# Kernel tuning notes

Measured on AMD Instinct MI355X. Metric: run time of the kernel, lower is better.

## Reference

```python
import jax, jax.numpy as jnp
import numpy as np

B, Cin, Cout = 2, 32, 16
D, H, W = 48, 64, 128
K = 3
EPS = 1e-5  # BatchNorm3d default eps


def setup_inputs() -> dict:
    key = jax.random.key(0)
    ks = jax.random.split(key, 6)
    return {
        "x": jax.random.normal(ks[0], (B, Cin, D, H, W), jnp.float32),
        "weight": jax.random.normal(ks[1], (Cout, Cin, K, K, K), jnp.float32) * 0.05,
        "gamma": jax.random.uniform(ks[2], (Cout,), jnp.float32, minval=0.5, maxval=1.5),
        "beta": jax.random.normal(ks[3], (Cout,), jnp.float32) * 0.1,
        "running_mean": jax.random.normal(ks[4], (Cout,), jnp.float32) * 0.1,
        "running_var": jax.random.uniform(ks[5], (Cout,), jnp.float32, minval=0.5, maxval=1.5),
    }


def _binarize(v):
    # forward: sign(v) in {-1, 0, +1}; backward (STE): hardtanh grad (pass-through on |v|<=1)
    clipped = jnp.clip(v, -1.0, 1.0)
    return clipped + jax.lax.stop_gradient(jnp.sign(v) - clipped)


def reference(x, weight, gamma, beta, running_mean, running_var):
    b, c, d, h, w = x.shape
    # trilinear upsample, scale (1,2,2), align_corners=False (half-pixel centers)
    x = jax.image.resize(x, (b, c, d, 2 * h, 2 * w), method="trilinear")
    # binarize activations and weights; XNOR-style per-output-channel scale alpha = mean|W|
    xb = _binarize(x)
    alpha = jnp.mean(jnp.abs(weight), axis=(1, 2, 3, 4), keepdims=True)  # [Cout,1,1,1,1]
    wb = _binarize(weight) * alpha
    y = jax.lax.conv_general_dilated(
        xb, wb,
        window_strides=(1, 1, 1),
        padding=[(1, 1), (1, 1), (1, 1)],
        dimension_numbers=("NCDHW", "OIDHW", "NCDHW"),
    )  # [B, Cout, D, 2H, 2W]
    # fused BatchNorm3d (inference form) + ReLU
    inv = gamma / jnp.sqrt(running_var + EPS)
    shift = beta - running_mean * inv
    y = y * inv[None, :, None, None, None] + shift[None, :, None, None, None]
    return jax.nn.relu(y)
```

## Files before the change

### kernel.cpp

```cpp
#include <hip/hip_runtime.h>
#include <hip/hip_bf16.h>
#include <stdint.h>

#define BB   2
#define CIN  32
#define COUT 16
#define DD   48
#define HIN  64
#define WIN  128
#define H2   128
#define W2   256
#define PLANE_WORDS (H2 * W2)

__global__ __launch_bounds__(512) void ibc3d_prep(
    const float* __restrict__ wgt, const float* __restrict__ gamma,
    const float* __restrict__ beta, const float* __restrict__ rmean,
    const float* __restrict__ rvar, uint32_t* __restrict__ bw,
    float* __restrict__ scale, float* __restrict__ shift)
{
    int t = threadIdx.x;
    if (t < 27 * 16) {
        int tap = t >> 4, co = t & 15;
        uint32_t word = 0;
        for (int ci = 0; ci < CIN; ++ci) {
            float v = wgt[(co * CIN + ci) * 27 + tap];
            word |= (v > 0.0f ? 1u : 0u) << ci;
        }
        bw[t] = word;
    } else if (t < 27 * 16 + 16) {
        int co = t - 27 * 16;
        double s = 0.0;
        for (int i = 0; i < CIN * 27; ++i)
            s += fabs((double)wgt[co * CIN * 27 + i]);
        float alpha = (float)(s / (double)(CIN * 27));
        float inv = gamma[co] / sqrtf(rvar[co] + 1e-5f);
        scale[co] = alpha * inv;
        shift[co] = beta[co] - rmean[co] * inv;
    }
}

__device__ __forceinline__ uint32_t pack_word(const float* __restrict__ x,
                                              int b, int d, int h2, int w2)
{
    int m = h2 >> 1, dh = h2 & 1;
    int n = w2 >> 1, dwp = w2 & 1;
    int rA = m + dh - 1;
    int rB = rA + 1;
    double wA = dh ? 0.75 : 0.25;
    double wB = 1.0 - wA;
    rA = rA < 0 ? 0 : rA;
    rB = rB > (HIN - 1) ? (HIN - 1) : rB;
    int cA = n + dwp - 1;
    int cB = cA + 1;
    double wC = dwp ? 0.75 : 0.25;
    double wD = 1.0 - wC;
    cA = cA < 0 ? 0 : cA;
    cB = cB > (WIN - 1) ? (WIN - 1) : cB;

    const float* xp = x + ((size_t)b * CIN * DD + d) * (HIN * WIN);
    int oA = rA * WIN, oB = rB * WIN;
    uint32_t word = 0;
    for (int ci = 0; ci < CIN; ++ci) {
        const float* xc = xp + (size_t)ci * (DD * HIN * WIN);
        float a0 = xc[oA + cA], a1 = xc[oA + cB];
        float b0 = xc[oB + cA], b1 = xc[oB + cB];
        double t0 = wA * (double)a0 + wB * (double)b0;
        double t1 = wA * (double)a1 + wB * (double)b1;
        double v  = wC * t0 + wD * t1;
        word |= (v >= 0.0 ? 1u : 0u) << ci;
    }
    return word;
}

__global__ __launch_bounds__(256) void ibc3d_packq8(
    const float* __restrict__ x, uint32_t* __restrict__ bx,
    int b_start, int nplanes)
{
    int idx = blockIdx.x * 256 + threadIdx.x;
    int j  = idx & 31;
    int m  = (idx >> 5) & 63;
    int pl = idx >> 11;
    if (pl >= nplanes) return;
    int d  = pl % DD;
    int b  = b_start + pl / DD;

    int rm1 = m > 0 ? m - 1 : 0;
    int rp1 = m < HIN - 1 ? m + 1 : HIN - 1;
    int c0  = 4 * j;
    int cl  = c0 >= 2 ? c0 - 2 : 0;
    int cr  = (c0 + 4 <= WIN - 2) ? c0 + 4 : WIN - 2;

    const float* xp = x + ((size_t)b * CIN * DD + d) * (HIN * WIN);
    int o0 = rm1 * WIN, o1 = m * WIN, o2 = rp1 * WIN;

    uint32_t w0[8], w1[8];
#pragma unroll
    for (int k = 0; k < 8; ++k) { w0[k] = 0u; w1[k] = 0u; }

#pragma unroll 2
    for (int ci = 0; ci < CIN; ++ci) {
        const float* xc = xp + (size_t)ci * (DD * HIN * WIN);
        float c[3][6];
#pragma unroll
        for (int r = 0; r < 3; ++r) {
            const float* row = xc + (r == 0 ? o0 : (r == 1 ? o1 : o2));
            float2 L = *(const float2*)(row + cl);
            float4 M = *(const float4*)(row + c0);
            float2 R = *(const float2*)(row + cr);
            c[r][0] = (j > 0)  ? L.y : L.x;
            c[r][1] = M.x; c[r][2] = M.y; c[r][3] = M.z; c[r][4] = M.w;
            c[r][5] = (j < 31) ? R.x : R.y;
        }

        float u[3][8];
#pragma unroll
        for (int r = 0; r < 3; ++r) {
#pragma unroll
            for (int t = 0; t < 4; ++t) {
                u[r][2 * t]     = 0.25f * c[r][t]     + 0.75f * c[r][t + 1];
                u[r][2 * t + 1] = 0.75f * c[r][t + 1] + 0.25f * c[r][t + 2];
            }
        }
        float v0[8], v1[8];
#pragma unroll
        for (int k = 0; k < 8; ++k) {
            v0[k] = 0.25f * u[0][k] + 0.75f * u[1][k];
            v1[k] = 0.75f * u[1][k] + 0.25f * u[2][k];
        }

        float amin = 3.4e38f;
#pragma unroll
        for (int k = 0; k < 8; ++k)
            amin = fminf(amin, fminf(fabsf(v0[k]), fabsf(v1[k])));

        if (__builtin_expect(amin < 1e-5f, 0)) {
            double e[3][8];
#pragma unroll
            for (int r = 0; r < 3; ++r) {
#pragma unroll
                for (int t = 0; t < 4; ++t) {
                    e[r][2 * t]     = 0.25 * (double)c[r][t]     + 0.75 * (double)c[r][t + 1];
                    e[r][2 * t + 1] = 0.75 * (double)c[r][t + 1] + 0.25 * (double)c[r][t + 2];
                }
            }
#pragma unroll
            for (int k = 0; k < 8; ++k) {
                uint32_t s0 = (0.25 * e[0][k] + 0.75 * e[1][k]) >= 0.0;
                uint32_t s1 = (0.75 * e[1][k] + 0.25 * e[2][k]) >= 0.0;
                w0[k] |= s0 << ci;
                w1[k] |= s1 << ci;
            }
        } else {
#pragma unroll
            for (int k = 0; k < 8; ++k) {
                uint32_t s0 = v0[k] >= 0.0f;
                uint32_t s1 = v1[k] >= 0.0f;
                w0[k] |= s0 << ci;
                w1[k] |= s1 << ci;
            }
        }
    }

    size_t base = (size_t)pl * PLANE_WORDS + (size_t)(2 * m) * W2 + 8 * j;
    *(uint4*)(bx + base)          = make_uint4(w0[0], w0[1], w0[2], w0[3]);
    *(uint4*)(bx + base + 4)      = make_uint4(w0[4], w0[5], w0[6], w0[7]);
    *(uint4*)(bx + base + W2)     = make_uint4(w1[0], w1[1], w1[2], w1[3]);
    *(uint4*)(bx + base + W2 + 4) = make_uint4(w1[4], w1[5], w1[6], w1[7]);
}

__global__ __launch_bounds__(256) void ibc3d_conv3(
    const uint32_t* __restrict__ bx, const uint32_t* __restrict__ bwg,
    const float* __restrict__ scaleg, const float* __restrict__ shiftg,
    float* __restrict__ out, int b_start)
{
    int bid   = blockIdx.x;
    int h2    = bid & (H2 - 1);
    int plane = bid >> 7;
    int d     = plane % DD;
    int b     = b_start + plane / DD;
    int w2    = threadIdx.x;

    int acc[16];
#pragma unroll
    for (int c = 0; c < 16; ++c) acc[c] = 0;

#pragma unroll
    for (int kd = 0; kd < 3; ++kd) {
        int dd = d + kd - 1;
        if (dd < 0 || dd >= DD) continue;
        const uint32_t* bxp = bx + (size_t)(plane + kd - 1) * PLANE_WORDS;
#pragma unroll
        for (int kh = 0; kh < 3; ++kh) {
            int hh = h2 + kh - 1;
            if (hh < 0 || hh >= H2) continue;
            const uint32_t* brow = bxp + hh * W2;
#pragma unroll
            for (int kw = 0; kw < 3; ++kw) {
                int ww = w2 + kw - 1;
                if (ww >= 0 && ww < W2) {
                    uint32_t word = brow[ww];
                    int tap = kd * 9 + kh * 3 + kw;
#pragma unroll
                    for (int co = 0; co < 16; ++co)
                        acc[co] += __popc(word ^ bwg[tap * 16 + co]);
                }
            }
        }
    }

    int nd = 1 + (d > 0)  + (d < DD - 1);
    int nh = 1 + (h2 > 0) + (h2 < H2 - 1);
    int nw = 1 + (w2 > 0) + (w2 < W2 - 1);
    float base = 32.0f * (float)(nd * nh * nw);

    size_t obase = (((size_t)(b * COUT) * DD + d) * H2 + h2) * W2 + w2;
#pragma unroll
    for (int co = 0; co < 16; ++co) {
        float y = (base - 2.0f * (float)acc[co]) * scaleg[co] + shiftg[co];
        y = y > 0.0f ? y : 0.0f;
        out[obase + (size_t)co * (DD * H2 * W2)] = y;
    }
}

__global__ __launch_bounds__(256) void ibc3d_fused(
    const float* __restrict__ x, const float* __restrict__ wgt,
    const float* __restrict__ gamma, const float* __restrict__ beta,
    const float* __restrict__ rmean, const float* __restrict__ rvar,
    float* __restrict__ out)
{
    __shared__ uint32_t sbw[27 * 16];
    __shared__ float sscale[16];
    __shared__ float sshift[16];
    __shared__ uint32_t sw[3][10][264];

    int tid = threadIdx.x;
    for (int t = tid; t < 27 * 16; t += 256) {
        int tap = t >> 4, co = t & 15;
        uint32_t word = 0;
        for (int ci = 0; ci < CIN; ++ci) {
            float v = wgt[(co * CIN + ci) * 27 + tap];
            word |= (v > 0.0f ? 1u : 0u) << ci;
        }
        sbw[t] = word;
    }
    if (tid < 16) {
        int co = tid;
        double s = 0.0;
        for (int i = 0; i < CIN * 27; ++i)
            s += fabs((double)wgt[co * CIN * 27 + i]);
        float alpha = (float)(s / (double)(CIN * 27));
        float inv = gamma[co] / sqrtf(rvar[co] + 1e-5f);
        sscale[co] = alpha * inv;
        sshift[co] = beta[co] - rmean[co] * inv;
    }

    int bid = blockIdx.x;
    int hq  = bid & 15;
    int r   = bid >> 4;
    int b   = r / DD;
    int d   = r % DD;
    int h2base = hq * 8;

    for (int i = tid; i < 3 * 10 * 258; i += 256) {
        int kd  = i / 2580;
        int rem = i - kd * 2580;
        int ri  = rem / 258;
        int ciw = rem - ri * 258;
        int dd = d + kd - 1;
        int h2 = h2base - 1 + ri;
        int w2 = ciw - 1;
        uint32_t word = 0;
        if (dd >= 0 && dd < DD && h2 >= 0 && h2 < H2 && w2 >= 0 && w2 < W2)
            word = pack_word(x, b, dd, h2, w2);
        sw[kd][ri][ciw] = word;
    }
    __syncthreads();

    int w2 = tid;
    for (int p = 0; p < 8; ++p) {
        int h2 = h2base + p;
        int acc[16];
#pragma unroll
        for (int c = 0; c < 16; ++c) acc[c] = 0;
        int nv = 0;
        for (int kd = 0; kd < 3; ++kd) {
            int dd = d + kd - 1;
            if (dd < 0 || dd >= DD) continue;
            for (int kh = 0; kh < 3; ++kh) {
                int hh = h2 + kh - 1;
                if (hh < 0 || hh >= H2) continue;
                for (int kw = 0; kw < 3; ++kw) {
                    int ww = w2 + kw - 1;
                    if (ww < 0 || ww >= W2) continue;
                    uint32_t word = sw[kd][p + kh][w2 + kw];
                    nv += 1;
                    int tap = kd * 9 + kh * 3 + kw;
#pragma unroll
                    for (int co = 0; co < 16; ++co)
                        acc[co] += __popc(word ^ sbw[tap * 16 + co]);
                }
            }
        }
        float base = 32.0f * (float)nv;
#pragma unroll
        for (int co = 0; co < 16; ++co) {
            float y = (base - 2.0f * (float)acc[co]) * sscale[co] + sshift[co];
            y = y > 0.0f ? y : 0.0f;
            size_t oidx = (((size_t)(b * COUT + co) * DD + d) * H2 + h2) * W2 + w2;
            out[oidx] = y;
        }
    }
}

extern "C" void kernel_launch(void* const* d_in, const int* in_sizes, int n_in,
                              void* d_out, int out_size, void* d_ws, size_t ws_size,
                              hipStream_t stream)
{
    (void)in_sizes; (void)n_in; (void)out_size;
    const float* x     = (const float*)d_in[0];
    const float* wgt   = (const float*)d_in[1];
    const float* gamma = (const float*)d_in[2];
    const float* beta  = (const float*)d_in[3];
    const float* rmean = (const float*)d_in[4];
    const float* rvar  = (const float*)d_in[5];
    float* out = (float*)d_out;

    const size_t HDR = 4096;
    const size_t bx_full = (size_t)BB * DD * PLANE_WORDS * 4;
    const size_t bx_half = (size_t)DD * PLANE_WORDS * 4;

    if (d_ws != nullptr && ws_size >= HDR + bx_full) {
        uint8_t* ws = (uint8_t*)d_ws;
        uint32_t* bw    = (uint32_t*)ws;
        float*    scale = (float*)(ws + 2048);
        float*    shift = (float*)(ws + 2112);
        uint32_t* bx    = (uint32_t*)(ws + HDR);
        ibc3d_prep<<<1, 512, 0, stream>>>(wgt, gamma, beta, rmean, rvar, bw, scale, shift);
        int nplanes = BB * DD;
        ibc3d_packq8<<<nplanes * 8, 256, 0, stream>>>(x, bx, 0, nplanes);
        ibc3d_conv3<<<nplanes * H2, 256, 0, stream>>>(bx, bw, scale, shift, out, 0);
    } else if (d_ws != nullptr && ws_size >= HDR + bx_half) {
        uint8_t* ws = (uint8_t*)d_ws;
        uint32_t* bw    = (uint32_t*)ws;
        float*    scale = (float*)(ws + 2048);
        float*    shift = (float*)(ws + 2112);
        uint32_t* bx    = (uint32_t*)(ws + HDR);
        ibc3d_prep<<<1, 512, 0, stream>>>(wgt, gamma, beta, rmean, rvar, bw, scale, shift);
        for (int b = 0; b < BB; ++b) {
            ibc3d_packq8<<<DD * 8, 256, 0, stream>>>(x, bx, b, DD);
            ibc3d_conv3<<<DD * H2, 256, 0, stream>>>(bx, bw, scale, shift, out, b);
        }
    } else {
        ibc3d_fused<<<BB * DD * (H2 / 8), 256, 0, stream>>>(
            x, wgt, gamma, beta, rmean, rvar, out);
    }
}
```

Measured before the change: 148.8 us.

## Split packing to one output row per thread, swizzle block order, warp-reduce alpha

The pack kernel now gives each thread a single upsampled output row instead of two, which doubles the grid and cuts per-thread register and load pressure, at the cost of reading each input row twice. Both the pack and conv kernels remap block indices with an 8-way interleave so that consecutive blocks are spread across the tensor, likely to balance work across XCDs or cache partitions. The prep kernel computes the per-channel alpha sum as a 32-lane parallel reduction with shuffles instead of a serial 864-element loop per thread. The changed summation order in double precision could shift alpha by a tiny rounding amount.

```diff
diff --git a/kernel.cpp b/kernel.cpp
--- a/kernel.cpp
+++ b/kernel.cpp
@@ -27,15 +27,22 @@
             word |= (v > 0.0f ? 1u : 0u) << ci;
         }
         bw[t] = word;
-    } else if (t < 27 * 16 + 16) {
-        int co = t - 27 * 16;
-        double s = 0.0;
-        for (int i = 0; i < CIN * 27; ++i)
-            s += fabs((double)wgt[co * CIN * 27 + i]);
-        float alpha = (float)(s / (double)(CIN * 27));
-        float inv = gamma[co] / sqrtf(rvar[co] + 1e-5f);
-        scale[co] = alpha * inv;
-        shift[co] = beta[co] - rmean[co] * inv;
+    }
+    {
+        int co   = t >> 5;
+        int lane = t & 31;
+        double p = 0.0;
+        for (int k = 0; k < 27; ++k)
+            p += fabs((double)wgt[co * (CIN * 27) + lane + 32 * k]);
+#pragma unroll
+        for (int s = 16; s >= 1; s >>= 1)
+            p += __shfl_down(p, s, 32);
+        if (lane == 0) {
+            float alpha = (float)(p / (double)(CIN * 27));
+            float inv = gamma[co] / sqrtf(rvar[co] + 1e-5f);
+            scale[co] = alpha * inv;
+            shift[co] = beta[co] - rmean[co] * inv;
+        }
     }
 }
 
@@ -72,108 +79,109 @@
     return word;
 }
 
-__global__ __launch_bounds__(256) void ibc3d_packq8(
+__global__ __launch_bounds__(256) void ibc3d_packr8(
     const float* __restrict__ x, uint32_t* __restrict__ bx,
     int b_start, int nplanes)
 {
-    int idx = blockIdx.x * 256 + threadIdx.x;
+    int per = gridDim.x >> 3;
+    int bid = (blockIdx.x & 7) * per + (blockIdx.x >> 3);
+    int idx = bid * 256 + threadIdx.x;
     int j  = idx & 31;
-    int m  = (idx >> 5) & 63;
-    int pl = idx >> 11;
+    int h2 = (idx >> 5) & (H2 - 1);
+    int pl = idx >> 12;
     if (pl >= nplanes) return;
     int d  = pl % DD;
     int b  = b_start + pl / DD;
 
-    int rm1 = m > 0 ? m - 1 : 0;
-    int rp1 = m < HIN - 1 ? m + 1 : HIN - 1;
-    int c0  = 4 * j;
-    int cl  = c0 >= 2 ? c0 - 2 : 0;
-    int cr  = (c0 + 4 <= WIN - 2) ? c0 + 4 : WIN - 2;
+    int m = h2 >> 1, q = h2 & 1;
+    int rT = q ? m : (m > 0 ? m - 1 : 0);
+    int rB = q ? (m < HIN - 1 ? m + 1 : HIN - 1) : m;
+    float wT = q ? 0.75f : 0.25f;
+    float wB = 1.0f - wT;
+
+    int c0 = 4 * j;
+    int cl = c0 >= 2 ? c0 - 2 : 0;
+    int cr = (c0 + 4 <= WIN - 2) ? c0 + 4 : WIN - 2;
 
     const float* xp = x + ((size_t)b * CIN * DD + d) * (HIN * WIN);
-    int o0 = rm1 * WIN, o1 = m * WIN, o2 = rp1 * WIN;
-
-    uint32_t w0[8], w1[8];
-#pragma unroll
-    for (int k = 0; k < 8; ++k) { w0[k] = 0u; w1[k] = 0u; }
+    int oT = rT * WIN, oB2 = rB * WIN;
+
+    uint32_t w[8];
+#pragma unroll
+    for (int k = 0; k < 8; ++k) w[k] = 0u;
 
 #pragma unroll 2
     for (int ci = 0; ci < CIN; ++ci) {
         const float* xc = xp + (size_t)ci * (DD * HIN * WIN);
-        float c[3][6];
-#pragma unroll
-        for (int r = 0; r < 3; ++r) {
-            const float* row = xc + (r == 0 ? o0 : (r == 1 ? o1 : o2));
-            float2 L = *(const float2*)(row + cl);
-            float4 M = *(const float4*)(row + c0);
-            float2 R = *(const float2*)(row + cr);
-            c[r][0] = (j > 0)  ? L.y : L.x;
-            c[r][1] = M.x; c[r][2] = M.y; c[r][3] = M.z; c[r][4] = M.w;
-            c[r][5] = (j < 31) ? R.x : R.y;
-        }
-
-        float u[3][8];
-#pragma unroll
-        for (int r = 0; r < 3; ++r) {
+        float cT[6], cB[6];
+        {
+            const float* rowT = xc + oT;
+            float2 L = *(const float2*)(rowT + cl);
+            float4 M = *(const float4*)(rowT + c0);
+            float2 R = *(const float2*)(rowT + cr);
+            cT[0] = (j > 0)  ? L.y : L.x;
+            cT[1] = M.x; cT[2] = M.y; cT[3] = M.z; cT[4] = M.w;
+            cT[5] = (j < 31) ? R.x : R.y;
+        }
+        {
+            const float* rowB = xc + oB2;
+            float2 L = *(const float2*)(rowB + cl);
+            float4 M = *(const float4*)(rowB + c0);
+            float2 R = *(const float2*)(rowB + cr);
+            cB[0] = (j > 0)  ? L.y : L.x;
+            cB[1] = M.x; cB[2] = M.y; cB[3] = M.z; cB[4] = M.w;
+            cB[5] = (j < 31) ? R.x : R.y;
+        }
+
+        float v[8];
+#pragma unroll
+        for (int t = 0; t < 4; ++t) {
+            float uT0 = 0.25f * cT[t]     + 0.75f * cT[t + 1];
+            float uT1 = 0.75f * cT[t + 1] + 0.25f * cT[t + 2];
+            float uB0 = 0.25f * cB[t]     + 0.75f * cB[t + 1];
+            float uB1 = 0.75f * cB[t + 1] + 0.25f * cB[t + 2];
+            v[2 * t]     = wT * uT0 + wB * uB0;
+            v[2 * t + 1] = wT * uT1 + wB * uB1;
+        }
+
+        float amin = 3.4e38f;
+#pragma unroll
+        for (int k = 0; k < 8; ++k)
+            amin = fminf(amin, fabsf(v[k]));
+
+        if (__builtin_expect(amin < 1e-5f, 0)) {
+            double dwT = (double)wT, dwB = 1.0 - (double)wT;
 #pragma unroll
             for (int t = 0; t < 4; ++t) {
-                u[r][2 * t]     = 0.25f * c[r][t]     + 0.75f * c[r][t + 1];
-                u[r][2 * t + 1] = 0.75f * c[r][t + 1] + 0.25f * c[r][t + 2];
-            }
-        }
-        float v0[8], v1[8];
-#pragma unroll
-        for (int k = 0; k < 8; ++k) {
-            v0[k] = 0.25f * u[0][k] + 0.75f * u[1][k];
-            v1[k] = 0.75f * u[1][k] + 0.25f * u[2][k];
-        }
-
-        float amin = 3.4e38f;
-#pragma unroll
-        for (int k = 0; k < 8; ++k)
-            amin = fminf(amin, fminf(fabsf(v0[k]), fabsf(v1[k])));
-
-        if (__builtin_expect(amin < 1e-5f, 0)) {
-            double e[3][8];
-#pragma unroll
-            for (int r = 0; r < 3; ++r) {
-#pragma unroll
-                for (int t = 0; t < 4; ++t) {
-                    e[r][2 * t]     = 0.25 * (double)c[r][t]     + 0.75 * (double)c[r][t + 1];
-                    e[r][2 * t + 1] = 0.75 * (double)c[r][t + 1] + 0.25 * (double)c[r][t + 2];
-                }
-            }
-#pragma unroll
-            for (int k = 0; k < 8; ++k) {
-                uint32_t s0 = (0.25 * e[0][k] + 0.75 * e[1][k]) >= 0.0;
-                uint32_t s1 = (0.75 * e[1][k] + 0.25 * e[2][k]) >= 0.0;
-                w0[k] |= s0 << ci;
-                w1[k] |= s1 << ci;
+                double eT0 = 0.25 * (double)cT[t]     + 0.75 * (double)cT[t + 1];
+                double eT1 = 0.75 * (double)cT[t + 1] + 0.25 * (double)cT[t + 2];
+                double eB0 = 0.25 * (double)cB[t]     + 0.75 * (double)cB[t + 1];
+                double eB1 = 0.75 * (double)cB[t + 1] + 0.25 * (double)cB[t + 2];
+                uint32_t s0 = (dwT * eT0 + dwB * eB0) >= 0.0;
+                uint32_t s1 = (dwT * eT1 + dwB * eB1) >= 0.0;
+                w[2 * t]     |= s0 << ci;
+                w[2 * t + 1] |= s1 << ci;
             }
         } else {
 #pragma unroll
-            for (int k = 0; k < 8; ++k) {
-                uint32_t s0 = v0[k] >= 0.0f;
-                uint32_t s1 = v1[k] >= 0.0f;
-                w0[k] |= s0 << ci;
-                w1[k] |= s1 << ci;
-            }
-        }
-    }
-
-    size_t base = (size_t)pl * PLANE_WORDS + (size_t)(2 * m) * W2 + 8 * j;
-    *(uint4*)(bx + base)          = make_uint4(w0[0], w0[1], w0[2], w0[3]);
-    *(uint4*)(bx + base + 4)      = make_uint4(w0[4], w0[5], w0[6], w0[7]);
-    *(uint4*)(bx + base + W2)     = make_uint4(w1[0], w1[1], w1[2], w1[3]);
-    *(uint4*)(bx + base + W2 + 4) = make_uint4(w1[4], w1[5], w1[6], w1[7]);
-}
-
-__global__ __launch_bounds__(256) void ibc3d_conv3(
+            for (int k = 0; k < 8; ++k)
+                w[k] |= (v[k] >= 0.0f ? 1u : 0u) << ci;
+        }
+    }
+
+    size_t base = (size_t)pl * PLANE_WORDS + (size_t)h2 * W2 + 8 * j;
+    *(uint4*)(bx + base)     = make_uint4(w[0], w[1], w[2], w[3]);
+    *(uint4*)(bx + base + 4) = make_uint4(w[4], w[5], w[6], w[7]);
+}
+
+__global__ __launch_bounds__(256) void ibc3d_conv6(
     const uint32_t* __restrict__ bx, const uint32_t* __restrict__ bwg,
     const float* __restrict__ scaleg, const float* __restrict__ shiftg,
     float* __restrict__ out, int b_start)
 {
-    int bid   = blockIdx.x;
+    int per = gridDim.x >> 3;
+    int bid = (blockIdx.x & 7) * per + (blockIdx.x >> 3);
+
     int h2    = bid & (H2 - 1);
     int plane = bid >> 7;
     int d     = plane % DD;
@@ -337,8 +345,8 @@
         uint32_t* bx    = (uint32_t*)(ws + HDR);
         ibc3d_prep<<<1, 512, 0, stream>>>(wgt, gamma, beta, rmean, rvar, bw, scale, shift);
         int nplanes = BB * DD;
-        ibc3d_packq8<<<nplanes * 8, 256, 0, stream>>>(x, bx, 0, nplanes);
-        ibc3d_conv3<<<nplanes * H2, 256, 0, stream>>>(bx, bw, scale, shift, out, 0);
+        ibc3d_packr8<<<nplanes * 16, 256, 0, stream>>>(x, bx, 0, nplanes);
+        ibc3d_conv6<<<nplanes * H2, 256, 0, stream>>>(bx, bw, scale, shift, out, 0);
     } else if (d_ws != nullptr && ws_size >= HDR + bx_half) {
         uint8_t* ws = (uint8_t*)d_ws;
         uint32_t* bw    = (uint32_t*)ws;
@@ -347,8 +355,8 @@
         uint32_t* bx    = (uint32_t*)(ws + HDR);
         ibc3d_prep<<<1, 512, 0, stream>>>(wgt, gamma, beta, rmean, rvar, bw, scale, shift);
         for (int b = 0; b < BB; ++b) {
-            ibc3d_packq8<<<DD * 8, 256, 0, stream>>>(x, bx, b, DD);
-            ibc3d_conv3<<<DD * H2, 256, 0, stream>>>(bx, bw, scale, shift, out, b);
+            ibc3d_packr8<<<DD * 16, 256, 0, stream>>>(x, bx, b, DD);
+            ibc3d_conv6<<<DD * H2, 256, 0, stream>>>(bx, bw, scale, shift, out, b);
         }
     } else {
         ibc3d_fused<<<BB * DD * (H2 / 8), 256, 0, stream>>>(
```

After: 146.7 us. Within noise of the previous version (-1.4%).
